# Kernel optimization log

Hardware: AMD Instinct MI355X
Metric: run time of the kernel (lower is better)

The kernel has to match this reference:

```python
import jax, jax.numpy as jnp
import numpy as np

B, S, D, VOCAB = 64, 2048, 256, 288

def setup_inputs() -> dict:
    key = jax.random.key(0)
    k1, k2, k3 = jax.random.split(key, 3)
    TE = jax.random.randint(k1, (B, S, 2), 0, VOCAB, dtype=jnp.int64)
    W1 = jax.random.normal(k2, (VOCAB + 7, D), dtype=jnp.float32) * 0.05
    b1 = jnp.zeros((D,), dtype=jnp.float32)
    W2 = jax.random.normal(k3, (D, D), dtype=jnp.float32) * 0.05
    b2 = jnp.zeros((D,), dtype=jnp.float32)
    return {"TE": TE, "T": VOCAB, "W1": W1, "b1": b1, "W2": W2, "b2": b2}

def reference(TE, T, W1, b1, W2, b2):
    # one_hot(day,7)||one_hot(time,T) @ W1  ==  gather rows of W1 and add
    day = TE[..., 0].astype(jnp.int32) % 7          # [B, S]
    tod = TE[..., 1].astype(jnp.int32) % T          # [B, S]
    h = W1[day] + W1[7 + tod] + b1                  # [B, S, D]  (Linear 1)
    h = jax.nn.relu(h)
    out = jnp.einsum('bsd,de->bse', h, W2) + b2     # [B, S, D]  (Linear 2)
    return out[:, :, None, :]                       # [B, S, 1, D]
```

## Files before the change

### kernel.cpp

```cpp
#include <hip/hip_runtime.h>
#include <hip/hip_bf16.h>


typedef __bf16 bf16x4 __attribute__((ext_vector_type(4)));
typedef __bf16 bf16x8 __attribute__((ext_vector_type(8)));
typedef float  f32x4  __attribute__((ext_vector_type(4)));

#define M_TOTAL   131072
#define BM        128


__global__ __launch_bounds__(64) void prep_all(const float* __restrict__ W1,
                                               const float* __restrict__ b1,
                                               const float* __restrict__ W2,
                                               __bf16* __restrict__ W2S,
                                               __bf16* __restrict__ Htab,
                                               const int* __restrict__ TE32,
                                               int* __restrict__ flag, int T) {
    const int b = blockIdx.x, lane = threadIdx.x;
    const int nTab = 7 * T;
    if (b < nTab) {
        const float* __restrict__ wa = W1 + (b / T) * 256;
        const float* __restrict__ wb = W1 + (7 + b % T) * 256;
        f32x4 a = *(const f32x4*)(wa + lane * 4);
        f32x4 c = *(const f32x4*)(wb + lane * 4);
        f32x4 d = *(const f32x4*)(b1 + lane * 4);
        bf16x4 h;
#pragma unroll
        for (int j = 0; j < 4; ++j) h[j] = (__bf16)fmaxf(a[j] + c[j] + d[j], 0.0f);
        *(bf16x4*)(Htab + b * 256 + lane * 4) = h;
    } else {
        const int wb = b - nTab;
#pragma unroll
        for (int q = 0; q < 2; ++q) {
            int c = (wb * 64 + lane) * 2 + q;
            int l = c & 63, ksnt = c >> 6;
            int ks = ksnt & 7, nt = ksnt >> 3;
            int n  = nt * 16 + (l & 15);
            int k0 = ks * 32 + (l >> 4) * 8;
            bf16x8 w;
#pragma unroll
            for (int j = 0; j < 8; ++j) w[j] = (__bf16)W2[(k0 + j) * 256 + n];
            *(bf16x8*)(W2S + c * 8) = w;
        }
        if (wb == 0) {
            int v = 0;
            for (int i = lane; i < 2048; i += 64) v |= TE32[2 * i + 1];
            unsigned long long nz = __ballot(v != 0);
            if (lane == 0) *flag = (nz == 0ull) ? 1 : 0;
        }
    }
}

__global__ __launch_bounds__(256, 3) void otab_gemm(
        const __bf16* __restrict__ Htab,
        const __bf16* __restrict__ W2S,
        const float* __restrict__ b2,
        float* __restrict__ Otab, int T)
{
    __shared__ __bf16 Bs[4 * 8 * 512];

    const int tid  = threadIdx.x;
    const int wave = tid >> 6;
    const int lane = tid & 63;
    const int m    = lane & 15;
    const int quad = lane >> 4;
    const int rowBase = blockIdx.x * BM + wave * 32;
    const int nTab = 7 * T;

    int code[2];
#pragma unroll
    for (int t = 0; t < 2; ++t) {
        int row = rowBase + t * 16 + m;
        code[t] = row < nTab ? row : nTab - 1;
    }
    bf16x8 hfrag[2][8];
#pragma unroll
    for (int t = 0; t < 2; ++t)
#pragma unroll
        for (int ks = 0; ks < 8; ++ks)
            hfrag[t][ks] = *(const bf16x8*)(Htab + code[t] * 256 + ks * 32 + quad * 8);

    const bf16x8* __restrict__ gsrc = (const bf16x8*)W2S + tid;
    bf16x8* __restrict__ ldst = (bf16x8*)Bs + tid;
    const bf16x8* __restrict__ lsrc = (const bf16x8*)Bs;

    bf16x8 stage[8];
#pragma unroll
    for (int q = 0; q < 8; ++q) stage[q] = gsrc[q * 256];

    for (int g = 0; g < 4; ++g) {
#pragma unroll
        for (int q = 0; q < 8; ++q) ldst[q * 256] = stage[q];
        __syncthreads();
        if (g < 3) {
#pragma unroll
            for (int q = 0; q < 8; ++q) stage[q] = gsrc[(g + 1) * 2048 + q * 256];
        }
#pragma unroll
        for (int ntl = 0; ntl < 4; ++ntl) {
            const int nt = g * 4 + ntl;
            f32x4 acc0 = {0.f, 0.f, 0.f, 0.f};
            f32x4 acc1 = {0.f, 0.f, 0.f, 0.f};
#pragma unroll
            for (int ks = 0; ks < 8; ++ks) {
                bf16x8 wfrag = lsrc[(ntl * 8 + ks) * 64 + lane];
                acc0 = __builtin_amdgcn_mfma_f32_16x16x32_bf16(wfrag, hfrag[0][ks], acc0, 0, 0, 0);
                acc1 = __builtin_amdgcn_mfma_f32_16x16x32_bf16(wfrag, hfrag[1][ks], acc1, 0, 0, 0);
            }
            const f32x4 bias = *(const f32x4*)(b2 + nt * 16 + quad * 4);
            f32x4 v0, v1;
#pragma unroll
            for (int r = 0; r < 4; ++r) { v0[r] = acc0[r] + bias[r]; v1[r] = acc1[r] + bias[r]; }
            float* p0 = Otab + (rowBase + m) * 256 + nt * 16 + quad * 4;
            *(f32x4*)p0 = v0;
            *(f32x4*)(p0 + 16 * 256) = v1;
        }
        __syncthreads();
    }
}

__global__ __launch_bounds__(256) void gather_out(
        const int*   __restrict__ TE32,
        const float* __restrict__ Otab,
        const int*   __restrict__ flag,
        float* __restrict__ out, int T)
{
    __shared__ int codes[64];
    const int tid  = threadIdx.x;
    const int wave = tid >> 6;
    const int lane = tid & 63;
    const int rowBase = blockIdx.x * 64;

    if (tid < 64) {
        const int is64 = *flag;
        const int row = rowBase + tid;
        int d32, t32;
        if (is64) { int4 te = *(const int4*)(TE32 + 4 * row); d32 = te.x; t32 = te.z; }
        else      { int2 te = *(const int2*)(TE32 + 2 * row); d32 = te.x; t32 = te.y; }
        int day = d32 % 7; if (day < 0) day += 7;
        int tod = t32 % T; if (tod < 0) tod += T;
        codes[tid] = day * T + tod;
    }
    __syncthreads();

    const float* src0 = Otab + lane * 4;
    float*       dst0 = out + (size_t)rowBase * 256 + (size_t)wave * 16 * 256 + lane * 4;
#pragma unroll
    for (int r = 0; r < 16; ++r) {
        const int c = codes[wave * 16 + r];
        f32x4 v = *(const f32x4*)(src0 + (size_t)c * 256);
        *(f32x4*)(dst0 + (size_t)r * 256) = v;
    }
}

__global__ __launch_bounds__(256, 3) void temb_gemm(
        const int*   __restrict__ TE32,
        const __bf16* __restrict__ Htab,
        const __bf16* __restrict__ W2S,
        const float* __restrict__ b2,
        const int*   __restrict__ flag,
        float* __restrict__ out, int T)
{
    __shared__ __bf16 Bs[4 * 8 * 512];

    const int is64 = *flag;
    const int tid  = threadIdx.x;
    const int wave = tid >> 6;
    const int lane = tid & 63;
    const int m    = lane & 15;
    const int quad = lane >> 4;
    const int rowBase = blockIdx.x * BM + wave * 32;

    int code[2];
#pragma unroll
    for (int t = 0; t < 2; ++t) {
        const int row = rowBase + t * 16 + m;
        int day, tod;
        if (is64) { int4 te = *(const int4*)(TE32 + 4 * row); day = te.x; tod = te.z; }
        else      { int2 te = *(const int2*)(TE32 + 2 * row); day = te.x; tod = te.y; }
        int dm = day % 7; if (dm < 0) dm += 7;
        int tm = tod % T; if (tm < 0) tm += T;
        code[t] = dm * T + tm;
    }
    bf16x8 hfrag[2][8];
#pragma unroll
    for (int t = 0; t < 2; ++t)
#pragma unroll
        for (int ks = 0; ks < 8; ++ks)
            hfrag[t][ks] = *(const bf16x8*)(Htab + code[t] * 256 + ks * 32 + quad * 8);

    const bf16x8* __restrict__ gsrc = (const bf16x8*)W2S + tid;
    bf16x8* __restrict__ ldst = (bf16x8*)Bs + tid;
    const bf16x8* __restrict__ lsrc = (const bf16x8*)Bs;

    bf16x8 stage[8];
#pragma unroll
    for (int q = 0; q < 8; ++q) stage[q] = gsrc[q * 256];

    for (int g = 0; g < 4; ++g) {
#pragma unroll
        for (int q = 0; q < 8; ++q) ldst[q * 256] = stage[q];
        __syncthreads();
        if (g < 3) {
#pragma unroll
            for (int q = 0; q < 8; ++q) stage[q] = gsrc[(g + 1) * 2048 + q * 256];
        }
#pragma unroll
        for (int ntl = 0; ntl < 4; ++ntl) {
            const int nt = g * 4 + ntl;
            f32x4 acc0 = {0.f, 0.f, 0.f, 0.f};
            f32x4 acc1 = {0.f, 0.f, 0.f, 0.f};
#pragma unroll
            for (int ks = 0; ks < 8; ++ks) {
                bf16x8 wfrag = lsrc[(ntl * 8 + ks) * 64 + lane];
                acc0 = __builtin_amdgcn_mfma_f32_16x16x32_bf16(wfrag, hfrag[0][ks], acc0, 0, 0, 0);
                acc1 = __builtin_amdgcn_mfma_f32_16x16x32_bf16(wfrag, hfrag[1][ks], acc1, 0, 0, 0);
            }
            const f32x4 bias = *(const f32x4*)(b2 + nt * 16 + quad * 4);
            f32x4 v0, v1;
#pragma unroll
            for (int r = 0; r < 4; ++r) { v0[r] = acc0[r] + bias[r]; v1[r] = acc1[r] + bias[r]; }
            float* p0 = out + (rowBase + m) * 256 + nt * 16 + quad * 4;
            *(f32x4*)p0 = v0;
            *(f32x4*)(p0 + 16 * 256) = v1;
        }
        __syncthreads();
    }
}

extern "C" void kernel_launch(void* const* d_in, const int* in_sizes, int n_in,
                              void* d_out, int out_size, void* d_ws, size_t ws_size,
                              hipStream_t stream) {
    const int*   TE = (const int*)  d_in[0];
    const float* W1 = (const float*)d_in[2];
    const float* b1 = (const float*)d_in[3];
    const float* W2 = (const float*)d_in[4];
    const float* b2 = (const float*)d_in[5];
    const int T = in_sizes[2] / 256 - 7;

    const int otab_blocks = (7 * T + BM - 1) / BM;
    const int otab_rows   = otab_blocks * BM;

    const size_t hoff = 131072;
    const size_t foff = hoff + (size_t)7 * T * 512;
    const size_t ooff = foff + 256;
    const size_t need = ooff + (size_t)otab_rows * 1024;

    __bf16* W2S  = (__bf16*)d_ws;
    __bf16* Htab = (__bf16*)((char*)d_ws + hoff);
    int*    flag = (int*)  ((char*)d_ws + foff);
    float*  Otab = (float*)((char*)d_ws + ooff);
    float*  out  = (float*)d_out;

    prep_all<<<7 * T + 64, 64, 0, stream>>>(W1, b1, W2, W2S, Htab, TE, flag, T);
    if (ws_size >= need) {
        otab_gemm<<<otab_blocks, 256, 0, stream>>>(Htab, W2S, b2, Otab, T);
        gather_out<<<M_TOTAL / 64, 256, 0, stream>>>(TE, Otab, flag, out, T);
    } else {
        temb_gemm<<<M_TOTAL / BM, 256, 0, stream>>>(TE, Htab, W2S, b2, flag, out, T);
    }
}
```

Before: 169.6 us.

## Fuse output-table GEMM and gather into one cooperative kernel with grid sync

Replaces the separate otab_gemm and gather_out launches with one cooperative kernel of 512 blocks. The first blocks compute the output table, all blocks decode their 256 row codes up front, and after a grid-wide sync each block gathers table rows into the output, staging 16 loads before the matching stores. This removes one kernel launch boundary and overlaps code decoding with the GEMM. In exchange it adds a grid barrier, a cooperative launch path, and lower occupancy per block (launch bounds of 2 instead of 3).

```diff
diff --git a/kernel.cpp b/kernel.cpp
--- a/kernel.cpp
+++ b/kernel.cpp
@@ -1,5 +1,8 @@
 #include <hip/hip_runtime.h>
 #include <hip/hip_bf16.h>
+#include <hip/hip_cooperative_groups.h>
+
+namespace cg = cooperative_groups;
 
 
 typedef __bf16 bf16x4 __attribute__((ext_vector_type(4)));
@@ -8,6 +11,7 @@
 
 #define M_TOTAL   131072
 #define BM        128
+#define FUSED_GRID 512
 
 
 __global__ __launch_bounds__(64) void prep_all(const float* __restrict__ W1,
@@ -52,20 +56,17 @@
     }
 }
 
-__global__ __launch_bounds__(256, 3) void otab_gemm(
-        const __bf16* __restrict__ Htab,
-        const __bf16* __restrict__ W2S,
-        const float* __restrict__ b2,
-        float* __restrict__ Otab, int T)
-{
-    __shared__ __bf16 Bs[4 * 8 * 512];
-
+__device__ __forceinline__ void otab_block_body(
+        const __bf16* __restrict__ Htab, const __bf16* __restrict__ W2S,
+        const float* __restrict__ b2, float* __restrict__ Otab, int T,
+        __bf16* Bs, int blk)
+{
     const int tid  = threadIdx.x;
+    const int lane = tid & 63;
     const int wave = tid >> 6;
-    const int lane = tid & 63;
     const int m    = lane & 15;
     const int quad = lane >> 4;
-    const int rowBase = blockIdx.x * BM + wave * 32;
+    const int rowBase = blk * BM + wave * 32;
     const int nTab = 7 * T;
 
     int code[2];
@@ -120,11 +121,65 @@
     }
 }
 
+__global__ __launch_bounds__(256, 2) void fused_otab_gather(
+        const int*   __restrict__ TE32,
+        const __bf16* __restrict__ Htab,
+        const __bf16* __restrict__ W2S,
+        const float* __restrict__ b2,
+        const int*   __restrict__ flag,
+        float* __restrict__ Otab,
+        float* __restrict__ out, int T)
+{
+    __shared__ __bf16 Bs[4 * 8 * 512];
+    __shared__ int codes[256];
+
+    const int tid  = threadIdx.x;
+    const int wave = tid >> 6;
+    const int lane = tid & 63;
+
+    {
+        const int is64 = *flag;
+        const int row = blockIdx.x * 256 + tid;
+        int d32, t32;
+        if (is64) { int4 te = *(const int4*)(TE32 + 4 * row); d32 = te.x; t32 = te.z; }
+        else      { int2 te = *(const int2*)(TE32 + 2 * row); d32 = te.x; t32 = te.y; }
+        int day = d32 % 7; if (day < 0) day += 7;
+        int tod = t32 % T; if (tod < 0) tod += T;
+        codes[tid] = day * T + tod;
+    }
+
+    const int otab_blocks = (7 * T + BM - 1) / BM;
+    if (blockIdx.x < otab_blocks)
+        otab_block_body(Htab, W2S, b2, Otab, T, Bs, blockIdx.x);
+
+    cg::this_grid().sync();
+
+    const float* srcB = Otab + lane * 4;
+    float* dstW = out + ((size_t)blockIdx.x * 256 + wave * 64) * 256 + lane * 4;
+#pragma unroll
+    for (int chunk = 0; chunk < 4; ++chunk) {
+        const int r0 = wave * 64 + chunk * 16;
+        f32x4 v[16];
+#pragma unroll
+        for (int r = 0; r < 16; ++r)
+            v[r] = *(const f32x4*)(srcB + (size_t)codes[r0 + r] * 256);
+#pragma unroll
+        for (int r = 0; r < 16; ++r)
+            *(f32x4*)(dstW + (size_t)(chunk * 16 + r) * 256) = v[r];
+    }
+}
+
+__global__ __launch_bounds__(256, 3) void otab_gemm(
+        const __bf16* __restrict__ Htab, const __bf16* __restrict__ W2S,
+        const float* __restrict__ b2, float* __restrict__ Otab, int T)
+{
+    __shared__ __bf16 Bs[4 * 8 * 512];
+    otab_block_body(Htab, W2S, b2, Otab, T, Bs, blockIdx.x);
+}
+
 __global__ __launch_bounds__(256) void gather_out(
-        const int*   __restrict__ TE32,
-        const float* __restrict__ Otab,
-        const int*   __restrict__ flag,
-        float* __restrict__ out, int T)
+        const int*   __restrict__ TE32, const float* __restrict__ Otab,
+        const int*   __restrict__ flag, float* __restrict__ out, int T)
 {
     __shared__ int codes[64];
     const int tid  = threadIdx.x;
@@ -155,12 +210,9 @@
 }
 
 __global__ __launch_bounds__(256, 3) void temb_gemm(
-        const int*   __restrict__ TE32,
-        const __bf16* __restrict__ Htab,
-        const __bf16* __restrict__ W2S,
-        const float* __restrict__ b2,
-        const int*   __restrict__ flag,
-        float* __restrict__ out, int T)
+        const int*   __restrict__ TE32, const __bf16* __restrict__ Htab,
+        const __bf16* __restrict__ W2S, const float* __restrict__ b2,
+        const int*   __restrict__ flag, float* __restrict__ out, int T)
 {
     __shared__ __bf16 Bs[4 * 8 * 512];
 
@@ -253,11 +305,34 @@
     float*  Otab = (float*)((char*)d_ws + ooff);
     float*  out  = (float*)d_out;
 
+    static int coop = -1;
+    if (coop < 0) {
+        int v = 0;
+        hipDeviceGetAttribute(&v, hipDeviceAttributeCooperativeLaunch, 0);
+        coop = v ? 1 : 0;
+    }
+
     prep_all<<<7 * T + 64, 64, 0, stream>>>(W1, b1, W2, W2S, Htab, TE, flag, T);
+
+    bool done = false;
     if (ws_size >= need) {
-        otab_gemm<<<otab_blocks, 256, 0, stream>>>(Htab, W2S, b2, Otab, T);
-        gather_out<<<M_TOTAL / 64, 256, 0, stream>>>(TE, Otab, flag, out, T);
-    } else {
+        if (coop) {
+            const int* TEa = TE; const __bf16* Ha = Htab; const __bf16* Wa = W2S;
+            const float* ba = b2; const int* fa = flag; float* Oa = Otab;
+            float* oa = out; int Ta = T;
+            void* args[] = {(void*)&TEa, (void*)&Ha, (void*)&Wa, (void*)&ba,
+                            (void*)&fa, (void*)&Oa, (void*)&oa, (void*)&Ta};
+            hipError_t e = hipLaunchCooperativeKernel((void*)fused_otab_gather,
+                                                      dim3(FUSED_GRID), dim3(256),
+                                                      args, 0, stream);
+            done = (e == hipSuccess);
+        }
+        if (!done) {
+            otab_gemm<<<otab_blocks, 256, 0, stream>>>(Htab, W2S, b2, Otab, T);
+            gather_out<<<M_TOTAL / 64, 256, 0, stream>>>(TE, Otab, flag, out, T);
+            done = true;
+        }
+    }
+    if (!done)
         temb_gemm<<<M_TOTAL / BM, 256, 0, stream>>>(TE, Htab, W2S, b2, flag, out, T);
-    }
-}
+}
```

Measured after the change: 234.2 us. 38.1% more time.
